# Optimization experiments

Measured on AMD Instinct MI355X. Metric: run time of the kernel, lower is better.

## Reference

```python
import jax, jax.numpy as jnp
import numpy as np

K, NC, NA = 9, 13, 5
NB, NH, NW = 128, 26, 26
NT, L = 50, 2 * K + 3
NOOBJ, OBJ, SIL = 1.0, 5.0, 0.6
COORD_S, CLASS_S = 1.0, 1.0
PRETRAIN_EPOCHS = 15
TH, SHARP = 80.0, 2.0                      # corner-conf distance threshold (px), sharpness
SCALE = np.array([640.0, 480.0], np.float32)  # im_width, im_height used by corner_confidences
CONF0 = float(np.exp(SHARP) - 1.0)
ANCHORS = np.array([1.482, 2.2412, 2.0501, 3.1265, 2.3946, 4.6891,
                    3.1018, 3.991, 3.4879, 5.8851], np.float32).reshape(NA, 2)


def setup_inputs():
    k1, k2 = jax.random.split(jax.random.key(0))
    output = jax.random.normal(k1, (NB, NA * (2 * K + 1 + NC), NH, NW), dtype=jnp.float32)
    target = jax.random.uniform(k2, (NB, NT * L), dtype=jnp.float32)
    return {"output": output, "target": target, "epoch": 20}


def _corner_conf(pred, gt):
    # pred, gt: [..., K, 2] normalized corners -> mean per-corner confidence [...]
    d = jnp.sqrt((((pred - gt) * jnp.asarray(SCALE)) ** 2).sum(-1))  # pixel distance [..., K]
    c = (jnp.exp(SHARP * (1.0 - d / TH)) - 1.0) / CONF0
    return jnp.where(d < TH, c, 0.0).mean(-1)


def _region_loss(output, target, epoch):
    nAnch, nPix = NA * NH * NW, NH * NW
    tgt = jax.lax.stop_gradient(target).reshape(NB, NT, L)
    out = output.reshape(NB, NA, 2 * K + 1 + NC, NH, NW)
    # keypoint 0 gets sigmoid, the rest are raw offsets
    xs = jnp.concatenate([jax.nn.sigmoid(out[:, :, 0:1]), out[:, :, 2:2 * K:2]], axis=2)  # [B,A,K,H,W]
    ys = jnp.concatenate([jax.nn.sigmoid(out[:, :, 1:2]), out[:, :, 3:2 * K:2]], axis=2)
    conf = jax.nn.sigmoid(out[:, :, 2 * K])                             # [B,A,H,W]
    cls_logits = jnp.transpose(out[:, :, 2 * K + 1:], (0, 1, 3, 4, 2))  # [B,A,H,W,NC]

    gxg = jnp.arange(NW, dtype=jnp.float32)
    gyg = jnp.arange(NH, dtype=jnp.float32)
    px = (jax.lax.stop_gradient(xs) + gxg) / NW            # detached, as torch uses .data
    py = (jax.lax.stop_gradient(ys) + gyg[:, None]) / NH
    # pred corners per anchor cell, flat anchor index = a*H*W + j*W + i -> [B, A*H*W, K, 2]
    pc = jnp.transpose(jnp.stack([px, py], -1), (0, 1, 3, 4, 2, 5)).reshape(NB, nAnch, K, 2)

    gt_xy = tgt[:, :, 1:1 + 2 * K].reshape(NB, NT, K, 2)
    # torch loop breaks at first target with x1 == 0 -> cumulative validity
    valid = jnp.cumprod((tgt[:, :, 1] != 0).astype(jnp.int32), axis=1) > 0  # [B,T]

    # pass 1: max corner confidence over valid GT, per anchor cell
    def max_conf_step(cur, inp):
        gt_t, v_t = inp                                    # [B,K,2], [B]
        c = _corner_conf(pc, gt_t[:, None]).reshape(NB, NA, NH, NW)
        return jnp.where(v_t[:, None, None, None], jnp.maximum(cur, c), cur), None

    cur_confs, _ = jax.lax.scan(max_conf_step, jnp.zeros((NB, NA, NH, NW), jnp.float32),
                                (jnp.swapaxes(gt_xy, 0, 1), valid.T))
    conf_mask0 = jnp.where(cur_confs > SIL, 0.0, NOOBJ)

    # per-target quantities (vectorized over b,t)
    gx = gt_xy[..., 0] * NW                                # [B,T,K]
    gy = gt_xy[..., 1] * NH
    gi0 = jnp.clip(jnp.floor(gx[:, :, 0]).astype(jnp.int32), 0, NW - 1)  # [B,T]
    gj0 = jnp.clip(jnp.floor(gy[:, :, 0]).astype(jnp.int32), 0, NH - 1)
    # pred_box is fetched with best_n == -1 (as in the source); emulate torch negative flat index via mod
    flat_idx = jnp.mod(jnp.arange(NB)[:, None] * nAnch - nPix + gj0 * NW + gi0, NB * nAnch)
    pred_box = pc.reshape(NB * nAnch, K, 2)[flat_idx]      # [B,T,K,2]
    conf_t = _corner_conf(pred_box, gt_xy)                 # [B,T]
    gw = tgt[:, :, L - 2] * NW
    gh = tgt[:, :, L - 1] * NH
    aw, ah = ANCHORS[:, 0], ANCHORS[:, 1]
    mw = jnp.minimum(aw, gw[..., None])                    # centered-box IoU (bbox_iou, cxcywh)
    mh = jnp.minimum(ah, gh[..., None])
    inter = mw * mh
    iou = inter / (aw * ah + (gw * gh)[..., None] - inter)
    best_n = jnp.argmax(iou, axis=-1).astype(jnp.int32)    # [B,T] (first max, like strict '>')
    txv = gx - gi0[..., None].astype(jnp.float32)          # [B,T,K]
    tyv = gy - gj0[..., None].astype(jnp.float32)
    tclsv = tgt[:, :, 0]

    # pass 2: sequential scatter matching torch overwrite order over t
    barange = jnp.arange(NB)
    z = jnp.zeros((NB, NA, NH, NW), jnp.float32)
    zk = jnp.zeros((NB, NA, NH, NW, K), jnp.float32)

    def scatter_step(carry, inp):
        cm, clm, cfm, tx, ty, tcf, tcl = carry
        v, bn, gj, gi, cft, txt, tyt, tct = inp
        idx = (barange, bn, gj, gi)
        vk = v[:, None]
        cm = cm.at[idx].set(jnp.where(v, 1.0, cm[idx]))
        clm = clm.at[idx].set(jnp.where(v, 1.0, clm[idx]))
        cfm = cfm.at[idx].set(jnp.where(v, OBJ, cfm[idx]))
        tx = tx.at[idx].set(jnp.where(vk, txt, tx[idx]))
        ty = ty.at[idx].set(jnp.where(vk, tyt, ty[idx]))
        tcf = tcf.at[idx].set(jnp.where(v, cft, tcf[idx]))
        tcl = tcl.at[idx].set(jnp.where(v, tct, tcl[idx]))
        return (cm, clm, cfm, tx, ty, tcf, tcl), None

    inps = (valid.T, best_n.T, gj0.T, gi0.T, conf_t.T,
            jnp.swapaxes(txv, 0, 1), jnp.swapaxes(tyv, 0, 1), tclsv.T)
    (coord_mask, cls_mask, conf_mask, tx, ty, tconf, tcls), _ = jax.lax.scan(
        scatter_step, (z, z, conf_mask0, zk, zk, z, z), inps)

    # losses
    xsT = jnp.transpose(xs, (0, 1, 3, 4, 2))               # [B,A,H,W,K]
    ysT = jnp.transpose(ys, (0, 1, 3, 4, 2))
    cmk = coord_mask[..., None]
    loss_x = 0.5 * COORD_S * jnp.sum(((xsT - tx) * cmk) ** 2)
    loss_y = 0.5 * COORD_S * jnp.sum(((ysT - ty) * cmk) ** 2)
    sq = jnp.sqrt(conf_mask)
    loss_conf = 0.5 * jnp.sum(((conf - tconf) * sq) ** 2)
    labels = jnp.clip(tcls.astype(jnp.int32), 0, NC - 1)
    ce = -jnp.take_along_axis(jax.nn.log_softmax(cls_logits, axis=-1),
                              labels[..., None], axis=-1)[..., 0]
    loss_cls = CLASS_S * jnp.sum(ce * cls_mask)
    loss = loss_x + loss_y + loss_cls
    if epoch > PRETRAIN_EPOCHS:
        loss = loss + loss_conf
    return loss


def reference(output, target, epoch):
    return _region_loss(output, target, epoch)
```

## Files before the change

kernel.cpp:

```cpp
#include <hip/hip_runtime.h>
#include <math.h>

#define KK     9
#define NCLS   13
#define NANC   5
#define NBB    128
#define NHH    26
#define NWW    26
#define NTT    50
#define LL     21
#define CHC    32
#define NPIX   676
#define NANCHT 3380
#define NCELLT 432640
#define GTS    20
#define TROWS  52
#define GTW    10
#define MWPB   106
#define HALFSPLIT 1792
#define NBLK   14

#define LOG2E_F   1.4426950408889634f
#define K1C       2.8853900817779268f
#define K2C       0.036067376022224085f
#define SXW       24.615384615384617f
#define SYH       18.461538461538463f
#define THRESH_S  43.500902934225507f
#define CULL_H    400.0f
#define CONF_T_SCALE 0.017390849194407297f
#define OBJ_W     5.0f
#define EPOCH_PRETRAIN 15
#define BIGV      6.0e18f
#define INFH      0x7C00u
#define INFH2     0x7C007C00u

typedef _Float16 h2 __attribute__((ext_vector_type(2)));

static __device__ __forceinline__ float fast_exp2(float x){ return __builtin_amdgcn_exp2f(x); }
static __device__ __forceinline__ float fast_sqrt(float x){ return __builtin_amdgcn_sqrtf(x); }
static __device__ __forceinline__ float sigmoidf_(float x){
  return 1.0f/(1.0f + fast_exp2(-LOG2E_F*x));
}
static __device__ __forceinline__ int pk_add_sv(int s, int v){
  int d; asm("v_pk_add_f16 %0, %1, %2" : "=v"(d) : "s"(s), "v"(v)); return d;
}
static __device__ __forceinline__ int pk_mul_vv(int a, int b){
  int d; asm("v_pk_mul_f16 %0, %1, %2" : "=v"(d) : "v"(a), "v"(b)); return d;
}
static __device__ __forceinline__ int pk_fma_vvv(int a, int b, int c){
  int d; asm("v_pk_fma_f16 %0, %1, %2, %3" : "=v"(d) : "v"(a), "v"(b), "v"(c)); return d;
}
static __device__ __forceinline__ int pk_min_vv(int a, int b){
  int d; asm("v_pk_min_f16 %0, %1, %2" : "=v"(d) : "v"(a), "v"(b)); return d;
}
static __device__ __forceinline__ unsigned short f2h_bits(float v){
  return __builtin_bit_cast(unsigned short, (_Float16)v);
}

__constant__ float c_anch[10] = {1.482f,2.2412f,2.0501f,3.1265f,2.3946f,4.6891f,
                                 3.1018f,3.991f,3.4879f,5.8851f};


__global__ __launch_bounds__(64) void prep_kernel(const float* __restrict__ tgt,
                                                  float* __restrict__ gts_neg,
                                                  unsigned* __restrict__ gthw,
                                                  int* __restrict__ nvalid){
  int b = blockIdx.x;
  int t = threadIdx.x;
  const float* trow = tgt + (size_t)b*NTT*LL;
  float v1 = (t < NTT) ? trow[t*LL + 1] : 0.0f;
  unsigned long long mk = __ballot(t < NTT && v1 != 0.0f);
  int nv = __ffsll(~mk) - 1;
  if (t == 0) nvalid[b] = nv;
  for (int idx = t; idx < NTT*GTS; idx += 64){
    int tt = idx / GTS;
    int c  = idx - tt*GTS;
    float v;
    if (c == 9 || c == 19)      v = BIGV;
    else if (c < 9)             v = -(trow[tt*LL + 1 + 2*c] * 640.0f);
    else                        v = -(trow[tt*LL + 2 + 2*(c-10)] * 480.0f);
    gts_neg[(size_t)b*NTT*GTS + idx] = v;
  }
  if (t < TROWS){
    unsigned w[GTW];
    if (t < nv){
      const float* tr = trow + t*LL;
      float xs[KK], ys[KK];
#pragma unroll
      for (int k = 0; k < KK; ++k){
        xs[k] = -(tr[1+2*k] * 640.0f);
        ys[k] = -(tr[2+2*k] * 480.0f);
      }
#pragma unroll
      for (int p = 0; p < 4; ++p){
        w[p]   = (unsigned)f2h_bits(xs[2*p]) | ((unsigned)f2h_bits(xs[2*p+1]) << 16);
        w[5+p] = (unsigned)f2h_bits(ys[2*p]) | ((unsigned)f2h_bits(ys[2*p+1]) << 16);
      }
      w[4] = (unsigned)f2h_bits(xs[8]) | (INFH << 16);
      w[9] = (unsigned)f2h_bits(ys[8]) | (INFH << 16);
    } else {
#pragma unroll
      for (int p = 0; p < GTW; ++p) w[p] = INFH2;
    }
    unsigned* dst = gthw + ((size_t)b*TROWS + t)*GTW;
#pragma unroll
    for (int p = 0; p < GTW; ++p) dst[p] = w[p];
  }
}

__global__ __launch_bounds__(128) void region_confmask_kernel(
    const float* __restrict__ outp, const unsigned* __restrict__ gthw,
    const float* __restrict__ gts_neg, unsigned int* __restrict__ maskw,
    double* __restrict__ partials){
  int b = blockIdx.y;
  int tid = threadIdx.x;
  int c0 = blockIdx.x * 128 + tid;
  int c1 = c0 + HALFSPLIT;
  bool ok1 = (c1 < NANCHT);

  __shared__ float sgt[NTT*GTS] __attribute__((aligned(16)));
  {
    const float* g32 = gts_neg + (size_t)b*NTT*GTS;
    for (int idx = tid; idx < NTT*GTS; idx += 128) sgt[idx] = g32[idx];
  }

  float Pxf0[KK], Pyf0[KK], Pxf1[KK], Pyf1[KK];
  int Pxw0[5], Pyw0[5], Pxw1[5], Pyw1[5];
  float cf0, cf1 = 0.0f;
  {
    int a = c0 / NPIX, rem = c0 - a*NPIX;
    int j = rem / NWW, i = rem - j*NWW;
    const float* base = outp + (((size_t)b*NANC + a)*CHC)*NPIX + rem;
#pragma unroll
    for (int k = 0; k < KK; ++k){
      float rx = base[(2*k)*NPIX], ry = base[(2*k+1)*NPIX];
      if (k == 0){ rx = sigmoidf_(rx); ry = sigmoidf_(ry); }
      Pxf0[k] = (rx + (float)i)*SXW; Pyf0[k] = (ry + (float)j)*SYH;
    }
    cf0 = sigmoidf_(base[(2*KK)*NPIX]);
  }
  if (ok1){
    int a = c1 / NPIX, rem = c1 - a*NPIX;
    int j = rem / NWW, i = rem - j*NWW;
    const float* base = outp + (((size_t)b*NANC + a)*CHC)*NPIX + rem;
#pragma unroll
    for (int k = 0; k < KK; ++k){
      float rx = base[(2*k)*NPIX], ry = base[(2*k+1)*NPIX];
      if (k == 0){ rx = sigmoidf_(rx); ry = sigmoidf_(ry); }
      Pxf1[k] = (rx + (float)i)*SXW; Pyf1[k] = (ry + (float)j)*SYH;
    }
    cf1 = sigmoidf_(base[(2*KK)*NPIX]);
  } else {
#pragma unroll
    for (int k = 0; k < KK; ++k){ Pxf1[k] = 0.0f; Pyf1[k] = 0.0f; }
  }
#pragma unroll
  for (int p = 0; p < 4; ++p){
    Pxw0[p] = (unsigned)f2h_bits(Pxf0[2*p]) | ((unsigned)f2h_bits(Pxf0[2*p+1]) << 16);
    Pyw0[p] = (unsigned)f2h_bits(Pyf0[2*p]) | ((unsigned)f2h_bits(Pyf0[2*p+1]) << 16);
    Pxw1[p] = (unsigned)f2h_bits(Pxf1[2*p]) | ((unsigned)f2h_bits(Pxf1[2*p+1]) << 16);
    Pyw1[p] = (unsigned)f2h_bits(Pyf1[2*p]) | ((unsigned)f2h_bits(Pyf1[2*p+1]) << 16);
  }
  Pxw0[4] = (unsigned)f2h_bits(Pxf0[8]); Pyw0[4] = (unsigned)f2h_bits(Pyf0[8]);
  Pxw1[4] = (unsigned)f2h_bits(Pxf1[8]); Pyw1[4] = (unsigned)f2h_bits(Pyf1[8]);
  __syncthreads();

  const _Float16 TH16 = (_Float16)CULL_H;
  const unsigned* gsrc = gthw + (size_t)b*TROWS*GTW;
  unsigned long long q0 = 0ull, q1 = 0ull;
#pragma unroll 1
  for (int c = 0; c < 13; ++c){
    int G[40];
#pragma unroll
    for (int w = 0; w < 40; ++w) G[w] = (int)gsrc[c*40 + w];
#pragma unroll
    for (int u = 0; u < 4; ++u){
      int t = c*4 + u;
      unsigned long long bit = 1ull << t;
      {
        int dx = pk_add_sv(G[u*10+0], Pxw0[0]); int r = pk_mul_vv(dx,dx);
        int dy = pk_add_sv(G[u*10+5], Pyw0[0]); r = pk_fma_vvv(dy,dy,r);
        int m = r;
#pragma unroll
        for (int p = 1; p < 5; ++p){
          dx = pk_add_sv(G[u*10+p],   Pxw0[p]); r = pk_mul_vv(dx,dx);
          dy = pk_add_sv(G[u*10+5+p], Pyw0[p]); r = pk_fma_vvv(dy,dy,r);
          m = pk_min_vv(m, r);
        }
        h2 mh = __builtin_bit_cast(h2, m);
        if ((mh[0] < TH16) | (mh[1] < TH16)) q0 |= bit;
      }
      {
        int dx = pk_add_sv(G[u*10+0], Pxw1[0]); int r = pk_mul_vv(dx,dx);
        int dy = pk_add_sv(G[u*10+5], Pyw1[0]); r = pk_fma_vvv(dy,dy,r);
        int m = r;
#pragma unroll
        for (int p = 1; p < 5; ++p){
          dx = pk_add_sv(G[u*10+p],   Pxw1[p]); r = pk_mul_vv(dx,dx);
          dy = pk_add_sv(G[u*10+5+p], Pyw1[p]); r = pk_fma_vvv(dy,dy,r);
          m = pk_min_vv(m, r);
        }
        h2 mh = __builtin_bit_cast(h2, m);
        if ((mh[0] < TH16) | (mh[1] < TH16)) q1 |= bit;
      }
    }
  }
  if (!ok1) q1 = 0ull;

  int m0_0 = 1, m0_1 = 1;
  {
    bool e0 = false, e1 = false;
    while (q0){
      int t = __ffsll((long long)q0) - 1; q0 &= q0 - 1;
      const float* gg = sgt + t*GTS;
      float s = 0.0f;
#pragma unroll
      for (int k = 0; k < KK; ++k){
        float dx = Pxf0[k] + gg[k], dy = Pyf0[k] + gg[10+k];
        float d  = fast_sqrt(fmaf(dy, dy, dx*dx));
        float e  = fast_exp2(fmaf(d, -K2C, K1C));
        s += fmaxf(e, 1.0f);
      }
      e0 |= (s > THRESH_S);
    }
    while (q1){
      int t = __ffsll((long long)q1) - 1; q1 &= q1 - 1;
      const float* gg = sgt + t*GTS;
      float s = 0.0f;
#pragma unroll
      for (int k = 0; k < KK; ++k){
        float dx = Pxf1[k] + gg[k], dy = Pyf1[k] + gg[10+k];
        float d  = fast_sqrt(fmaf(dy, dy, dx*dx));
        float e  = fast_exp2(fmaf(d, -K2C, K1C));
        s += fmaxf(e, 1.0f);
      }
      e1 |= (s > THRESH_S);
    }
    if (e0) m0_0 = 0;
    if (e1) m0_1 = 0;
  }

  float contrib = (m0_0 ? 0.5f*cf0*cf0 : 0.0f) + ((ok1 && m0_1) ? 0.5f*cf1*cf1 : 0.0f);

  int lane = tid & 63;
  int wavebase0 = blockIdx.x * 128 + (tid & ~63);
  unsigned long long mb0 = __ballot(m0_0 != 0);
  if ((lane & 31) == 0){
    unsigned int w = (lane == 0) ? (unsigned int)mb0 : (unsigned int)(mb0 >> 32);
    maskw[(size_t)b*MWPB + (wavebase0 >> 5) + (lane >> 5)] = w;
  }
  unsigned long long mb1 = __ballot(m0_1 != 0);
  int wavebase1 = wavebase0 + HALFSPLIT;
  if ((lane & 31) == 0 && wavebase1 < NANCHT){
    unsigned int w = (lane == 0) ? (unsigned int)mb1 : (unsigned int)(mb1 >> 32);
    maskw[(size_t)b*MWPB + (wavebase1 >> 5) + (lane >> 5)] = w;
  }

#pragma unroll
  for (int o = 32; o > 0; o >>= 1) contrib += __shfl_xor(contrib, o, 64);
  __shared__ float wsum[2];
  int wid = tid >> 6;
  if (lane == 0) wsum[wid] = contrib;
  __syncthreads();
  if (tid == 0)
    partials[b*NBLK + blockIdx.x] = (double)wsum[0] + (double)wsum[1];
}

__global__ __launch_bounds__(64) void scatter_loss_kernel(
    const float* __restrict__ outp, const float* __restrict__ tgt,
    const int* __restrict__ nvalid, const unsigned int* __restrict__ maskw,
    double* __restrict__ bc_part){
  int b = blockIdx.x;
  int t = threadIdx.x;
  __shared__ int keys[NTT];
  int nv = nvalid[b];
  bool valid = (t < nv);

  int key = -1, gi0 = 0, gj0 = 0, bn = 0;
  float txv[KK], tyv[KK];
  float conf_t = 0.0f, tcls = 0.0f;

  if (t < NTT){
    const float* trow = tgt + ((size_t)b*NTT + t)*LL;
    tcls = trow[0];
    float gx0 = trow[1]*(float)NWW;
    float gy0 = trow[2]*(float)NHH;
    gi0 = min(max((int)floorf(gx0), 0), NWW-1);
    gj0 = min(max((int)floorf(gy0), 0), NHH-1);
#pragma unroll
    for (int k = 0; k < KK; ++k){
      txv[k] = trow[1+2*k]*(float)NWW - (float)gi0;
      tyv[k] = trow[2+2*k]*(float)NHH - (float)gj0;
    }
    float gw = trow[LL-2]*(float)NWW, gh = trow[LL-1]*(float)NHH;
    float best = -1.0f;
    for (int a = 0; a < NANC; ++a){
      float aw = c_anch[2*a], ah = c_anch[2*a+1];
      float inter = fminf(aw, gw) * fminf(ah, gh);
      float iou = inter / (aw*ah + gw*gh - inter);
      if (iou > best){ best = iou; bn = a; }
    }
    key = bn*NPIX + gj0*NWW + gi0;
    keys[t] = key;

    long f = (long)b*NANCHT - NPIX + gj0*NWW + gi0;
    if (f < 0) f += NCELLT;
    int bb  = (int)(f / NANCHT);
    int rr  = (int)(f - (long)bb*NANCHT);
    int aa  = rr / NPIX;
    int rr2 = rr - aa*NPIX;
    int jj  = rr2 / NWW;
    int ii  = rr2 - jj*NWW;
    const float* pbase = outp + (((size_t)bb*NANC + aa)*CHC)*NPIX + rr2;
    float s = 0.0f;
#pragma unroll
    for (int k = 0; k < KK; ++k){
      float rx = pbase[(2*k)*NPIX], ry = pbase[(2*k+1)*NPIX];
      if (k == 0){ rx = sigmoidf_(rx); ry = sigmoidf_(ry); }
      float Pxx = (rx + (float)ii)*SXW, Pyy = (ry + (float)jj)*SYH;
      float dx = Pxx - trow[1+2*k]*640.0f;
      float dy = Pyy - trow[2+2*k]*480.0f;
      float d  = fast_sqrt(fmaf(dy, dy, dx*dx));
      float e  = fast_exp2(fmaf(d, -K2C, K1C));
      s += fmaxf(e, 1.0f);
    }
    conf_t = (s - 9.0f) * CONF_T_SCALE;
  }
  __syncthreads();

  bool winner = valid;
  if (valid){
    for (int u = t+1; u < nv; ++u) if (keys[u] == key){ winner = false; break; }
  }

  double lx = 0.0, ly = 0.0, lcls = 0.0, lcf = 0.0;
  if (winner){
    const float* cbase = outp + (((size_t)b*NANC + bn)*CHC)*NPIX + gj0*NWW + gi0;
    float sx = 0.0f, sy = 0.0f;
#pragma unroll
    for (int k = 0; k < KK; ++k){
      float rx = cbase[(2*k)*NPIX], ry = cbase[(2*k+1)*NPIX];
      if (k == 0){ rx = sigmoidf_(rx); ry = sigmoidf_(ry); }
      float dx = rx - txv[k], dy = ry - tyv[k];
      sx = fmaf(dx, dx, sx); sy = fmaf(dy, dy, sy);
    }
    lx = 0.5*(double)sx; ly = 0.5*(double)sy;

    float lg[NCLS], mx = -1e30f;
#pragma unroll
    for (int c = 0; c < NCLS; ++c){ lg[c] = cbase[(2*KK+1+c)*NPIX]; mx = fmaxf(mx, lg[c]); }
    float se = 0.0f;
#pragma unroll
    for (int c = 0; c < NCLS; ++c) se += fast_exp2((lg[c]-mx)*LOG2E_F);
    int label = min(max((int)tcls, 0), NCLS-1);
    lcls = (double)(mx + logf(se) - lg[label]);

    float cf = sigmoidf_(cbase[(2*KK)*NPIX]);
    int idx = bn*NPIX + gj0*NWW + gi0;
    int m0 = (maskw[(size_t)b*MWPB + (idx >> 5)] >> (idx & 31)) & 1;
    float dcf = cf - conf_t;
    lcf = 0.5*OBJ_W*(double)(dcf*dcf) - (m0 ? 0.5*(double)(cf*cf) : 0.0);
  }

#pragma unroll
  for (int o = 32; o > 0; o >>= 1){
    lx  += __shfl_xor(lx,  o, 64);
    ly  += __shfl_xor(ly,  o, 64);
    lcls+= __shfl_xor(lcls,o, 64);
    lcf += __shfl_xor(lcf, o, 64);
  }
  if (threadIdx.x == 0){
    double* bp = bc_part + (size_t)b*4;
    bp[0] = lx; bp[1] = ly; bp[2] = lcls; bp[3] = lcf;
  }
}

__global__ __launch_bounds__(256) void finalize_kernel(
    const double* __restrict__ bc_part, const double* __restrict__ partials,
    const int* __restrict__ epoch_p, float* __restrict__ outv){
  int tid = threadIdx.x;
  double vx=0, vy=0, vc=0, vf=0, vb=0;
  for (int i = tid; i < NBB; i += 256){
    vx += bc_part[4*i]; vy += bc_part[4*i+1];
    vc += bc_part[4*i+2]; vf += bc_part[4*i+3];
  }
  for (int i = tid; i < NBLK*NBB; i += 256) vb += partials[i];
#pragma unroll
  for (int o = 32; o > 0; o >>= 1){
    vx += __shfl_xor(vx, o, 64); vy += __shfl_xor(vy, o, 64);
    vc += __shfl_xor(vc, o, 64); vf += __shfl_xor(vf, o, 64);
    vb += __shfl_xor(vb, o, 64);
  }
  __shared__ double sm[5][4];
  int wid = tid >> 6, lane = tid & 63;
  if (lane == 0){ sm[0][wid]=vx; sm[1][wid]=vy; sm[2][wid]=vc; sm[3][wid]=vf; sm[4][wid]=vb; }
  __syncthreads();
  if (tid == 0){
    double fx=0, fy=0, fc=0, ff=0, fb=0;
    for (int w = 0; w < 4; ++w){ fx+=sm[0][w]; fy+=sm[1][w]; fc+=sm[2][w]; ff+=sm[3][w]; fb+=sm[4][w]; }
    double loss = fx + fy + fc;
    if (*epoch_p > EPOCH_PRETRAIN) loss += ff + fb;
    outv[0] = (float)loss;
  }
}

extern "C" void kernel_launch(void* const* d_in, const int* in_sizes, int n_in,
                              void* d_out, int out_size, void* d_ws, size_t ws_size,
                              hipStream_t stream){
  (void)in_sizes; (void)n_in; (void)out_size; (void)ws_size;
  const float* outp = (const float*)d_in[0];
  const float* tgt  = (const float*)d_in[1];
  const int*   ep   = (const int*)d_in[2];
  float* outv = (float*)d_out;
  char* ws = (char*)d_ws;

  double* bc_part   = (double*)(ws);
  double* partials  = (double*)(ws + 4096);
  float*  gts_neg   = (float*) (ws + 18432);
  int*    nvalid    = (int*)   (ws + 530432);
  unsigned int* maskw = (unsigned int*)(ws + 530944);
  unsigned* gthw    = (unsigned*)(ws + 585216);

  prep_kernel<<<dim3(NBB), dim3(64), 0, stream>>>(tgt, gts_neg, gthw, nvalid);
  region_confmask_kernel<<<dim3(NBLK, NBB), dim3(128), 0, stream>>>(outp, gthw, gts_neg, maskw, partials);
  scatter_loss_kernel<<<dim3(NBB), dim3(64), 0, stream>>>(outp, tgt, nvalid, maskw, bc_part);
  finalize_kernel<<<dim3(1), dim3(256), 0, stream>>>(bc_part, partials, ep, outv);
}
```

Baseline: 142.7 us.

## Tighten fp16 culling test, drop shared GT staging, recompute fp32 corners lazily

The packed fp16 cull test changes from a per-corner minimum-distance check to a sum of clamped (d^2 - 6400) terms compared against a negative threshold. This is a tighter bound on the summed corner confidence, so fewer targets should need the exact fp32 check. The shared-memory staging of the GT corners and the __syncthreads are removed. The fp32 predicted corners are no longer kept in registers; they are reloaded from global memory only when a wave has candidate targets, which cuts register pressure. The risk is that the fp16 sum bound must stay conservative: a missed target would give a wrong mask, and the global reloads add latency on the slow path.

```diff
diff --git a/kernel.cpp b/kernel.cpp
--- a/kernel.cpp
+++ b/kernel.cpp
@@ -26,13 +26,14 @@
 #define SXW       24.615384615384617f
 #define SYH       18.461538461538463f
 #define THRESH_S  43.500902934225507f
-#define CULL_H    400.0f
 #define CONF_T_SCALE 0.017390849194407297f
 #define OBJ_W     5.0f
 #define EPOCH_PRETRAIN 15
 #define BIGV      6.0e18f
 #define INFH      0x7C00u
 #define INFH2     0x7C007C00u
+#define NEG6400W  0xEE40EE40
+#define CULL_FIRE_NEG  -31000.0f
 
 typedef _Float16 h2 __attribute__((ext_vector_type(2)));
 
@@ -43,6 +44,9 @@
 }
 static __device__ __forceinline__ int pk_add_sv(int s, int v){
   int d; asm("v_pk_add_f16 %0, %1, %2" : "=v"(d) : "s"(s), "v"(v)); return d;
+}
+static __device__ __forceinline__ int pk_add_vv(int a, int b){
+  int d; asm("v_pk_add_f16 %0, %1, %2" : "=v"(d) : "v"(a), "v"(b)); return d;
 }
 static __device__ __forceinline__ int pk_mul_vv(int a, int b){
   int d; asm("v_pk_mul_f16 %0, %1, %2" : "=v"(d) : "v"(a), "v"(b)); return d;
@@ -118,24 +122,25 @@
   int c1 = c0 + HALFSPLIT;
   bool ok1 = (c1 < NANCHT);
 
-  __shared__ float sgt[NTT*GTS] __attribute__((aligned(16)));
-  {
-    const float* g32 = gts_neg + (size_t)b*NTT*GTS;
-    for (int idx = tid; idx < NTT*GTS; idx += 128) sgt[idx] = g32[idx];
-  }
-
-  float Pxf0[KK], Pyf0[KK], Pxf1[KK], Pyf1[KK];
   int Pxw0[5], Pyw0[5], Pxw1[5], Pyw1[5];
   float cf0, cf1 = 0.0f;
   {
     int a = c0 / NPIX, rem = c0 - a*NPIX;
     int j = rem / NWW, i = rem - j*NWW;
     const float* base = outp + (((size_t)b*NANC + a)*CHC)*NPIX + rem;
+    unsigned short hx[10], hy[10];
 #pragma unroll
     for (int k = 0; k < KK; ++k){
       float rx = base[(2*k)*NPIX], ry = base[(2*k+1)*NPIX];
       if (k == 0){ rx = sigmoidf_(rx); ry = sigmoidf_(ry); }
-      Pxf0[k] = (rx + (float)i)*SXW; Pyf0[k] = (ry + (float)j)*SYH;
+      hx[k] = f2h_bits((rx + (float)i)*SXW);
+      hy[k] = f2h_bits((ry + (float)j)*SYH);
+    }
+    hx[9] = 0; hy[9] = 0;
+#pragma unroll
+    for (int p = 0; p < 5; ++p){
+      Pxw0[p] = (int)((unsigned)hx[2*p] | ((unsigned)hx[2*p+1] << 16));
+      Pyw0[p] = (int)((unsigned)hy[2*p] | ((unsigned)hy[2*p+1] << 16));
     }
     cf0 = sigmoidf_(base[(2*KK)*NPIX]);
   }
@@ -143,29 +148,28 @@
     int a = c1 / NPIX, rem = c1 - a*NPIX;
     int j = rem / NWW, i = rem - j*NWW;
     const float* base = outp + (((size_t)b*NANC + a)*CHC)*NPIX + rem;
+    unsigned short hx[10], hy[10];
 #pragma unroll
     for (int k = 0; k < KK; ++k){
       float rx = base[(2*k)*NPIX], ry = base[(2*k+1)*NPIX];
       if (k == 0){ rx = sigmoidf_(rx); ry = sigmoidf_(ry); }
-      Pxf1[k] = (rx + (float)i)*SXW; Pyf1[k] = (ry + (float)j)*SYH;
+      hx[k] = f2h_bits((rx + (float)i)*SXW);
+      hy[k] = f2h_bits((ry + (float)j)*SYH);
+    }
+    hx[9] = 0; hy[9] = 0;
+#pragma unroll
+    for (int p = 0; p < 5; ++p){
+      Pxw1[p] = (int)((unsigned)hx[2*p] | ((unsigned)hx[2*p+1] << 16));
+      Pyw1[p] = (int)((unsigned)hy[2*p] | ((unsigned)hy[2*p+1] << 16));
     }
     cf1 = sigmoidf_(base[(2*KK)*NPIX]);
   } else {
 #pragma unroll
-    for (int k = 0; k < KK; ++k){ Pxf1[k] = 0.0f; Pyf1[k] = 0.0f; }
-  }
-#pragma unroll
-  for (int p = 0; p < 4; ++p){
-    Pxw0[p] = (unsigned)f2h_bits(Pxf0[2*p]) | ((unsigned)f2h_bits(Pxf0[2*p+1]) << 16);
-    Pyw0[p] = (unsigned)f2h_bits(Pyf0[2*p]) | ((unsigned)f2h_bits(Pyf0[2*p+1]) << 16);
-    Pxw1[p] = (unsigned)f2h_bits(Pxf1[2*p]) | ((unsigned)f2h_bits(Pxf1[2*p+1]) << 16);
-    Pyw1[p] = (unsigned)f2h_bits(Pyf1[2*p]) | ((unsigned)f2h_bits(Pyf1[2*p+1]) << 16);
-  }
-  Pxw0[4] = (unsigned)f2h_bits(Pxf0[8]); Pyw0[4] = (unsigned)f2h_bits(Pyf0[8]);
-  Pxw1[4] = (unsigned)f2h_bits(Pxf1[8]); Pyw1[4] = (unsigned)f2h_bits(Pyf1[8]);
-  __syncthreads();
-
-  const _Float16 TH16 = (_Float16)CULL_H;
+    for (int p = 0; p < 5; ++p){ Pxw1[p] = 0; Pyw1[p] = 0; }
+  }
+
+  const int negC = (int)NEG6400W;
+  const int zeroW = 0;
   const unsigned* gsrc = gthw + (size_t)b*TROWS*GTW;
   unsigned long long q0 = 0ull, q1 = 0ull;
 #pragma unroll 1
@@ -175,69 +179,100 @@
     for (int w = 0; w < 40; ++w) G[w] = (int)gsrc[c*40 + w];
 #pragma unroll
     for (int u = 0; u < 4; ++u){
-      int t = c*4 + u;
-      unsigned long long bit = 1ull << t;
+      unsigned long long bit = 1ull << (c*4 + u);
       {
-        int dx = pk_add_sv(G[u*10+0], Pxw0[0]); int r = pk_mul_vv(dx,dx);
-        int dy = pk_add_sv(G[u*10+5], Pyw0[0]); r = pk_fma_vvv(dy,dy,r);
-        int m = r;
-#pragma unroll
-        for (int p = 1; p < 5; ++p){
-          dx = pk_add_sv(G[u*10+p],   Pxw0[p]); r = pk_mul_vv(dx,dx);
-          dy = pk_add_sv(G[u*10+5+p], Pyw0[p]); r = pk_fma_vvv(dy,dy,r);
-          m = pk_min_vv(m, r);
+        int acc = zeroW;
+#pragma unroll
+        for (int p = 0; p < 5; ++p){
+          int dx = pk_add_sv(G[u*10+p],   Pxw0[p]);
+          int dy = pk_add_sv(G[u*10+5+p], Pyw0[p]);
+          int r2 = pk_mul_vv(dx, dx);
+          r2 = pk_fma_vvv(dy, dy, r2);
+          int um = pk_add_vv(r2, negC);
+          um = pk_min_vv(um, zeroW);
+          acc = pk_add_vv(acc, um);
         }
-        h2 mh = __builtin_bit_cast(h2, m);
-        if ((mh[0] < TH16) | (mh[1] < TH16)) q0 |= bit;
+        h2 ah = __builtin_bit_cast(h2, acc);
+        float s = (float)ah[0] + (float)ah[1];
+        if (s < CULL_FIRE_NEG) q0 |= bit;
       }
       {
-        int dx = pk_add_sv(G[u*10+0], Pxw1[0]); int r = pk_mul_vv(dx,dx);
-        int dy = pk_add_sv(G[u*10+5], Pyw1[0]); r = pk_fma_vvv(dy,dy,r);
-        int m = r;
-#pragma unroll
-        for (int p = 1; p < 5; ++p){
-          dx = pk_add_sv(G[u*10+p],   Pxw1[p]); r = pk_mul_vv(dx,dx);
-          dy = pk_add_sv(G[u*10+5+p], Pyw1[p]); r = pk_fma_vvv(dy,dy,r);
-          m = pk_min_vv(m, r);
+        int acc = zeroW;
+#pragma unroll
+        for (int p = 0; p < 5; ++p){
+          int dx = pk_add_sv(G[u*10+p],   Pxw1[p]);
+          int dy = pk_add_sv(G[u*10+5+p], Pyw1[p]);
+          int r2 = pk_mul_vv(dx, dx);
+          r2 = pk_fma_vvv(dy, dy, r2);
+          int um = pk_add_vv(r2, negC);
+          um = pk_min_vv(um, zeroW);
+          acc = pk_add_vv(acc, um);
         }
-        h2 mh = __builtin_bit_cast(h2, m);
-        if ((mh[0] < TH16) | (mh[1] < TH16)) q1 |= bit;
+        h2 ah = __builtin_bit_cast(h2, acc);
+        float s = (float)ah[0] + (float)ah[1];
+        if (s < CULL_FIRE_NEG) q1 |= bit;
       }
     }
   }
   if (!ok1) q1 = 0ull;
 
   int m0_0 = 1, m0_1 = 1;
-  {
-    bool e0 = false, e1 = false;
-    while (q0){
-      int t = __ffsll((long long)q0) - 1; q0 &= q0 - 1;
-      const float* gg = sgt + t*GTS;
-      float s = 0.0f;
+  if (__any((q0 | q1) != 0ull)){
+    const float* gbase = gts_neg + (size_t)b*NTT*GTS;
+    if (q0){
+      int a = c0 / NPIX, rem = c0 - a*NPIX;
+      int j = rem / NWW, i = rem - j*NWW;
+      const float* base = outp + (((size_t)b*NANC + a)*CHC)*NPIX + rem;
+      float Pxf[KK], Pyf[KK];
 #pragma unroll
       for (int k = 0; k < KK; ++k){
-        float dx = Pxf0[k] + gg[k], dy = Pyf0[k] + gg[10+k];
-        float d  = fast_sqrt(fmaf(dy, dy, dx*dx));
-        float e  = fast_exp2(fmaf(d, -K2C, K1C));
-        s += fmaxf(e, 1.0f);
-      }
-      e0 |= (s > THRESH_S);
-    }
-    while (q1){
-      int t = __ffsll((long long)q1) - 1; q1 &= q1 - 1;
-      const float* gg = sgt + t*GTS;
-      float s = 0.0f;
+        float rx = base[(2*k)*NPIX], ry = base[(2*k+1)*NPIX];
+        if (k == 0){ rx = sigmoidf_(rx); ry = sigmoidf_(ry); }
+        Pxf[k] = (rx + (float)i)*SXW; Pyf[k] = (ry + (float)j)*SYH;
+      }
+      bool exc = false;
+      while (q0){
+        int t = __ffsll((long long)q0) - 1; q0 &= q0 - 1;
+        const float* gg = gbase + t*GTS;
+        float s = 0.0f;
+#pragma unroll
+        for (int k = 0; k < KK; ++k){
+          float dx = Pxf[k] + gg[k], dy = Pyf[k] + gg[10+k];
+          float d  = fast_sqrt(fmaf(dy, dy, dx*dx));
+          float e  = fast_exp2(fmaf(d, -K2C, K1C));
+          s += fmaxf(e, 1.0f);
+        }
+        exc |= (s > THRESH_S);
+      }
+      if (exc) m0_0 = 0;
+    }
+    if (q1){
+      int a = c1 / NPIX, rem = c1 - a*NPIX;
+      int j = rem / NWW, i = rem - j*NWW;
+      const float* base = outp + (((size_t)b*NANC + a)*CHC)*NPIX + rem;
+      float Pxf[KK], Pyf[KK];
 #pragma unroll
       for (int k = 0; k < KK; ++k){
-        float dx = Pxf1[k] + gg[k], dy = Pyf1[k] + gg[10+k];
-        float d  = fast_sqrt(fmaf(dy, dy, dx*dx));
-        float e  = fast_exp2(fmaf(d, -K2C, K1C));
-        s += fmaxf(e, 1.0f);
-      }
-      e1 |= (s > THRESH_S);
-    }
-    if (e0) m0_0 = 0;
-    if (e1) m0_1 = 0;
+        float rx = base[(2*k)*NPIX], ry = base[(2*k+1)*NPIX];
+        if (k == 0){ rx = sigmoidf_(rx); ry = sigmoidf_(ry); }
+        Pxf[k] = (rx + (float)i)*SXW; Pyf[k] = (ry + (float)j)*SYH;
+      }
+      bool exc = false;
+      while (q1){
+        int t = __ffsll((long long)q1) - 1; q1 &= q1 - 1;
+        const float* gg = gbase + t*GTS;
+        float s = 0.0f;
+#pragma unroll
+        for (int k = 0; k < KK; ++k){
+          float dx = Pxf[k] + gg[k], dy = Pyf[k] + gg[10+k];
+          float d  = fast_sqrt(fmaf(dy, dy, dx*dx));
+          float e  = fast_exp2(fmaf(d, -K2C, K1C));
+          s += fmaxf(e, 1.0f);
+        }
+        exc |= (s > THRESH_S);
+      }
+      if (exc) m0_1 = 0;
+    }
   }
 
   float contrib = (m0_0 ? 0.5f*cf0*cf0 : 0.0f) + ((ok1 && m0_1) ? 0.5f*cf1*cf1 : 0.0f);
```

Result: no change. 140.3 us (-1.7%).
